# Kernel tuning notes

Measured on AMD Instinct MI355X. Metric: run time of the kernel, lower is better.

## Reference

```python
import jax, jax.numpy as jnp
import numpy as np

N_NODES = 50000
N_EDGES = 800000
D_IN = 128
D_OUT = 128


def setup_inputs() -> dict:
    key = jax.random.key(0)
    k1, k2, k3, k4, k5 = jax.random.split(key, 5)
    x = jax.random.normal(k1, (N_NODES, D_IN), dtype=jnp.float32)
    weight = jax.random.normal(k2, (D_IN, D_OUT), dtype=jnp.float32)
    bias = jax.random.normal(k3, (D_OUT,), dtype=jnp.float32)
    vals = jax.random.uniform(k4, (N_EDGES,), dtype=jnp.float32)
    row = jax.random.randint(k5, (N_EDGES,), 0, N_NODES, dtype=jnp.int32)
    col = jax.random.randint(jax.random.fold_in(k5, 1), (N_EDGES,), 0, N_NODES, dtype=jnp.int32)
    return {"x": x, "weight": weight, "bias": bias, "vals": vals, "row": row, "col": col}


def reference(x, weight, bias, vals, row, col):
    # Dense feature transform: x @ W   [N, D_out]
    h = x @ weight
    # SpMM: out[i] = sum_{e: row[e]==i} vals[e] * h[col[e]]
    msg = vals[:, None] * h[col]  # [E, D_out]
    out = jax.ops.segment_sum(msg, row, num_segments=N_NODES)
    # Fused bias + ReLU (original: out += bias; relu(out))
    out = jax.nn.relu(out + bias)
    return out
```

## Files before the change

### kernel.cpp

```cpp
#include <hip/hip_runtime.h>

#define N_NODES 50000
#define N_EDGES 800000
#define D 128
#define D4 32
#define D2 64

#define BIN_LOG 6
#define BIN_ROWS 64
#define NBINS ((N_NODES + BIN_ROWS - 1) / BIN_ROWS)
#define CAP 1280

#define CNT_STRIDE 16

#define NKEYS 512

#define GEMM_BLOCKS ((N_NODES + 63) / 64)
#define EPB 4096
#define PART_BLOCKS ((N_EDGES + EPB - 1) / EPB)
#define E4 (N_EDGES / 4)

typedef __attribute__((ext_vector_type(8))) short bf16x8;
typedef __attribute__((ext_vector_type(4))) float f32x4;

__device__ __forceinline__ unsigned bf16_1(float a) {
    unsigned u = __float_as_uint(a);
    return (u + 0x7fffu + ((u >> 16) & 1u)) >> 16;
}
__device__ __forceinline__ unsigned pack_bf16(float a, float b) {
    return bf16_1(a) | (bf16_1(b) << 16);
}
__device__ __forceinline__ float ubf_lo(unsigned u) {
    return __uint_as_float(u << 16);
}
__device__ __forceinline__ float ubf_hi(unsigned u) {
    return __uint_as_float(u & 0xffff0000u);
}

__global__ __launch_bounds__(256) void prep_and_zero(const float* __restrict__ w,
                                                     unsigned* __restrict__ wtu,
                                                     int4* __restrict__ cnt4) {
    const int i = blockIdx.x * 256 + threadIdx.x;
    if (i < (NBINS * CNT_STRIDE) / 4) cnt4[i] = make_int4(0, 0, 0, 0);
    if (i < D * 64) {
        const int col = i >> 6;
        const int k2  = i & 63;
        wtu[i] = pack_bf16(w[(size_t)(2 * k2) * D + col],
                           w[(size_t)(2 * k2 + 1) * D + col]);
    }
}

__global__ __launch_bounds__(256) void fused_gemm_partition(
        const float4* __restrict__ x4, const uint4* __restrict__ wt4,
        ushort* __restrict__ hb,
        const int4* __restrict__ rowi4, const int4* __restrict__ coli4,
        const float4* __restrict__ vals4,
        int* __restrict__ bin_cnt, uint2* __restrict__ bins) {

    if (blockIdx.x < PART_BLOCKS) {
        __shared__ int hist[NBINS];
        __shared__ int bbase[NBINS];
        const int base4 = blockIdx.x * (EPB / 4);

        for (int i = threadIdx.x; i < NBINS; i += 256) hist[i] = 0;
        __syncthreads();

        union { int4 v4[4]; int a[16]; } R, C;
        union { float4 v4[4]; float a[16]; } V;
        #pragma unroll
        for (int q = 0; q < 4; ++q) {
            const int i4  = base4 + q * 256 + threadIdx.x;
            const int i4c = (i4 < E4) ? i4 : (E4 - 1);
            R.v4[q] = rowi4[i4c];
            C.v4[q] = coli4[i4c];
            V.v4[q] = vals4[i4c];
            if (i4 >= E4) R.v4[q] = make_int4(-1, -1, -1, -1);
        }

        #pragma unroll
        for (int q = 0; q < 16; ++q)
            if (R.a[q] >= 0) atomicAdd(&hist[R.a[q] >> BIN_LOG], 1);
        __syncthreads();

        for (int i = threadIdx.x; i < NBINS; i += 256) {
            const int c = hist[i];
            bbase[i] = (c > 0) ? atomicAdd(&bin_cnt[i * CNT_STRIDE], c) : 0;
            hist[i] = 0;
        }
        __syncthreads();

        #pragma unroll
        for (int q = 0; q < 16; ++q) {
            const int r = R.a[q];
            if (r >= 0) {
                const int b = r >> BIN_LOG;
                const int k = bbase[b] + atomicAdd(&hist[b], 1);
                const unsigned c = (unsigned)C.a[q];
                if (k < CAP)
                    bins[(size_t)b * CAP + k] =
                        make_uint2((c << 16) | bf16_1(V.a[q]),
                                   ((unsigned)(r & (BIN_ROWS - 1)) << 3) | (c >> 13));
            }
        }
        return;
    }

    const int bid  = blockIdx.x - PART_BLOCKS;
    const int lane = threadIdx.x & 63;
    const int r0   = bid * 64 + (threadIdx.x >> 6) * 16;
    const int arow = r0 + (lane & 15);
    const int kg   = lane >> 4;
    const bool rok = (arow < N_NODES);

    bf16x8 afr[4];
    #pragma unroll
    for (int kc = 0; kc < 4; ++kc) {
        float4 f0 = make_float4(0.f, 0.f, 0.f, 0.f);
        float4 f1 = f0;
        if (rok) {
            const int c4 = kc * 8 + kg * 2;
            f0 = x4[(size_t)arow * D4 + c4];
            f1 = x4[(size_t)arow * D4 + c4 + 1];
        }
        union { bf16x8 v; unsigned u[4]; } a;
        a.u[0] = pack_bf16(f0.x, f0.y);
        a.u[1] = pack_bf16(f0.z, f0.w);
        a.u[2] = pack_bf16(f1.x, f1.y);
        a.u[3] = pack_bf16(f1.z, f1.w);
        afr[kc] = a.v;
    }

    f32x4 acc[8];
    #pragma unroll
    for (int t = 0; t < 8; ++t) acc[t] = (f32x4){0.f, 0.f, 0.f, 0.f};

    #pragma unroll
    for (int t = 0; t < 8; ++t) {
        const int col = t * 16 + (lane & 15);
        #pragma unroll
        for (int kc = 0; kc < 4; ++kc) {
            union { bf16x8 v; uint4 u; } b;
            b.u = wt4[(size_t)col * 16 + kc * 4 + kg];
            acc[t] = __builtin_amdgcn_mfma_f32_16x16x32_bf16(afr[kc], b.v,
                                                             acc[t], 0, 0, 0);
        }
    }

    #pragma unroll
    for (int t = 0; t < 8; ++t) {
        const int col = t * 16 + (lane & 15);
        #pragma unroll
        for (int j = 0; j < 4; ++j) {
            const int r = r0 + (lane >> 4) * 4 + j;
            if (r < N_NODES)
                hb[(size_t)r * D + col] = (ushort)bf16_1(acc[t][j]);
        }
    }
}

__global__ __launch_bounds__(512) void sort_gather(const int* __restrict__ bin_cnt,
                                                   const uint2* __restrict__ bins,
                                                   const uint2* __restrict__ hb2,
                                                   const float4* __restrict__ bias4,
                                                   float4* __restrict__ out4) {
    __shared__ int      hcnt[NKEYS];
    __shared__ int      cur[NKEYS];
    __shared__ int      starts[NKEYS + 1];
    __shared__ int      wsum[8], woff[8];
    __shared__ unsigned sorted[CAP];

    const int bin = blockIdx.x;
    const int tid = threadIdx.x;
    int n = bin_cnt[bin * CNT_STRIDE];
    n = (n > CAP) ? CAP : n;
    const uint2* brec = bins + (size_t)bin * CAP;

    if (tid < NKEYS) { hcnt[tid] = 0; cur[tid] = 0; }
    __syncthreads();

    for (int i = tid; i < n; i += 512) atomicAdd(&hcnt[brec[i].y], 1);
    __syncthreads();

    {
        int v = hcnt[tid];
        #pragma unroll
        for (int off = 1; off < 64; off <<= 1) {
            const int t = __shfl_up(v, off);
            if ((tid & 63) >= off) v += t;
        }
        starts[tid + 1] = v;
        if ((tid & 63) == 63) wsum[tid >> 6] = v;
    }
    __syncthreads();
    if (tid == 0) {
        int run = 0;
        #pragma unroll
        for (int w2 = 0; w2 < 8; ++w2) { woff[w2] = run; run += wsum[w2]; }
        starts[0] = 0;
    }
    __syncthreads();
    starts[tid + 1] += woff[tid >> 6];
    __syncthreads();

    for (int i = tid; i < n; i += 512) {
        const uint2 rec = brec[i];
        const int k = atomicAdd(&cur[rec.y], 1);
        sorted[starts[rec.y] + k] = rec.x;
    }
    __syncthreads();

    const int wave = tid >> 6;
    const int lane = tid & 63;
    const int half = lane >> 5;
    const int hl   = lane & 31;
    const float4 b = bias4[hl];

    #pragma unroll
    for (int rp = 0; rp < 4; ++rp) {
        const int row  = wave + 16 * rp + 8 * half;
        const int node = bin * BIN_ROWS + row;
        int s = 0, len = 0;
        if (node < N_NODES) {
            s   = starts[row << 3];
            len = starts[(row << 3) + 8] - s;
        }
        int lm = len;
        lm = max(lm, __shfl_xor(lm, 32));

        float4 acc = {0.f, 0.f, 0.f, 0.f};
        for (int j0 = 0; j0 < lm; j0 += 8) {
            uint2 hv[8];
            float vv[8];
            #pragma unroll
            for (int q = 0; q < 8; ++q) {
                const int jq = j0 + q;
                const int jj = (jq < len) ? (s + jq) : 0;
                unsigned ed = sorted[jj];
                ed = (jq < len) ? ed : 0u;
                vv[q] = __uint_as_float((ed & 0xffffu) << 16);
                hv[q] = hb2[(size_t)(ed >> 16) * 32 + hl];
            }
            #pragma unroll
            for (int q = 0; q < 8; ++q) {
                acc.x = fmaf(vv[q], ubf_lo(hv[q].x), acc.x);
                acc.y = fmaf(vv[q], ubf_hi(hv[q].x), acc.y);
                acc.z = fmaf(vv[q], ubf_lo(hv[q].y), acc.z);
                acc.w = fmaf(vv[q], ubf_hi(hv[q].y), acc.w);
            }
        }
        if (node < N_NODES) {
            float4 o;
            o.x = fmaxf(acc.x + b.x, 0.f);
            o.y = fmaxf(acc.y + b.y, 0.f);
            o.z = fmaxf(acc.z + b.z, 0.f);
            o.w = fmaxf(acc.w + b.w, 0.f);
            out4[(size_t)node * 32 + hl] = o;
        }
    }
}

extern "C" void kernel_launch(void* const* d_in, const int* in_sizes, int n_in,
                              void* d_out, int out_size, void* d_ws, size_t ws_size,
                              hipStream_t stream) {
    const float* x      = (const float*)d_in[0];
    const float* weight = (const float*)d_in[1];
    const float* bias   = (const float*)d_in[2];
    const float* vals   = (const float*)d_in[3];
    const int*   rowi   = (const int*)d_in[4];
    const int*   coli   = (const int*)d_in[5];
    float* out = (float*)d_out;

    char* w = (char*)d_ws;
    ushort*   hb      = (ushort*)w;   w += (size_t)N_NODES * D * sizeof(ushort);
    unsigned* wt      = (unsigned*)w; w += (size_t)D * 64 * sizeof(unsigned);
    int*      bin_cnt = (int*)w;      w += ((size_t)NBINS * CNT_STRIDE + 16) * sizeof(int);
    uint2*    bins    = (uint2*)w;

    prep_and_zero<<<32, 256, 0, stream>>>(weight, wt, (int4*)bin_cnt);

    fused_gemm_partition<<<PART_BLOCKS + GEMM_BLOCKS, 256, 0, stream>>>(
        (const float4*)x, (const uint4*)wt, hb,
        (const int4*)rowi, (const int4*)coli, (const float4*)vals,
        bin_cnt, bins);

    sort_gather<<<NBINS, 512, 0, stream>>>(bin_cnt, bins, (const uint2*)hb,
                                           (const float4*)bias, (float4*)out);
}
```

Before: 73.39 us.

## Replace global atomic edge binning with per-chunk local sort and bin gather

Each edge chunk is now counting-sorted by bin entirely in shared memory and written out contiguously, along with per-chunk bin start offsets. The sort_gather kernel scans those offsets across all chunks, prefix-sums them, and uses a binary search to fetch its records. This removes the global atomics on bin counters and the zeroing pass, and splits the fused GEMM/partition launch into two separate kernels. In exchange, every bin block reads a strided offset per chunk and does a binary search per record, partition and GEMM no longer overlap within one launch, and bins larger than CAP are no longer clamped.

```diff
diff --git a/kernel.cpp b/kernel.cpp
--- a/kernel.cpp
+++ b/kernel.cpp
@@ -11,14 +11,13 @@
 #define NBINS ((N_NODES + BIN_ROWS - 1) / BIN_ROWS)
 #define CAP 1280
 
-#define CNT_STRIDE 16
-
 #define NKEYS 512
 
+#define EPB 4096
+#define NCHUNK ((N_EDGES + EPB - 1) / EPB)
 #define GEMM_BLOCKS ((N_NODES + 63) / 64)
-#define EPB 4096
-#define PART_BLOCKS ((N_EDGES + EPB - 1) / EPB)
 #define E4 (N_EDGES / 4)
+#define STRIDE_ST (NBINS + 2)
 
 typedef __attribute__((ext_vector_type(8))) short bf16x8;
 typedef __attribute__((ext_vector_type(4))) float f32x4;
@@ -37,11 +36,9 @@
     return __uint_as_float(u & 0xffff0000u);
 }
 
-__global__ __launch_bounds__(256) void prep_and_zero(const float* __restrict__ w,
-                                                     unsigned* __restrict__ wtu,
-                                                     int4* __restrict__ cnt4) {
+__global__ __launch_bounds__(256) void prep_wt(const float* __restrict__ w,
+                                               unsigned* __restrict__ wtu) {
     const int i = blockIdx.x * 256 + threadIdx.x;
-    if (i < (NBINS * CNT_STRIDE) / 4) cnt4[i] = make_int4(0, 0, 0, 0);
     if (i < D * 64) {
         const int col = i >> 6;
         const int k2  = i & 63;
@@ -50,64 +47,96 @@
     }
 }
 
-__global__ __launch_bounds__(256) void fused_gemm_partition(
-        const float4* __restrict__ x4, const uint4* __restrict__ wt4,
-        ushort* __restrict__ hb,
+__global__ __launch_bounds__(256) void partition_edges(
         const int4* __restrict__ rowi4, const int4* __restrict__ coli4,
         const float4* __restrict__ vals4,
-        int* __restrict__ bin_cnt, uint2* __restrict__ bins) {
-
-    if (blockIdx.x < PART_BLOCKS) {
-        __shared__ int hist[NBINS];
-        __shared__ int bbase[NBINS];
-        const int base4 = blockIdx.x * (EPB / 4);
-
-        for (int i = threadIdx.x; i < NBINS; i += 256) hist[i] = 0;
-        __syncthreads();
-
-        union { int4 v4[4]; int a[16]; } R, C;
-        union { float4 v4[4]; float a[16]; } V;
-        #pragma unroll
-        for (int q = 0; q < 4; ++q) {
-            const int i4  = base4 + q * 256 + threadIdx.x;
-            const int i4c = (i4 < E4) ? i4 : (E4 - 1);
-            R.v4[q] = rowi4[i4c];
-            C.v4[q] = coli4[i4c];
-            V.v4[q] = vals4[i4c];
-            if (i4 >= E4) R.v4[q] = make_int4(-1, -1, -1, -1);
-        }
-
-        #pragma unroll
-        for (int q = 0; q < 16; ++q)
-            if (R.a[q] >= 0) atomicAdd(&hist[R.a[q] >> BIN_LOG], 1);
-        __syncthreads();
-
-        for (int i = threadIdx.x; i < NBINS; i += 256) {
-            const int c = hist[i];
-            bbase[i] = (c > 0) ? atomicAdd(&bin_cnt[i * CNT_STRIDE], c) : 0;
-            hist[i] = 0;
-        }
-        __syncthreads();
-
-        #pragma unroll
-        for (int q = 0; q < 16; ++q) {
-            const int r = R.a[q];
-            if (r >= 0) {
-                const int b = r >> BIN_LOG;
-                const int k = bbase[b] + atomicAdd(&hist[b], 1);
-                const unsigned c = (unsigned)C.a[q];
-                if (k < CAP)
-                    bins[(size_t)b * CAP + k] =
-                        make_uint2((c << 16) | bf16_1(V.a[q]),
-                                   ((unsigned)(r & (BIN_ROWS - 1)) << 3) | (c >> 13));
-            }
-        }
-        return;
-    }
-
-    const int bid  = blockIdx.x - PART_BLOCKS;
+        uint2* __restrict__ blk_rec, ushort* __restrict__ blk_starts) {
+    __shared__ int   hist[NBINS];
+    __shared__ int   sts[NBINS + 1];
+    __shared__ int   wsum[4], woff[4];
+    __shared__ uint2 recs[EPB];
+    const int tid = threadIdx.x;
+
+    for (int i = tid; i < NBINS; i += 256) hist[i] = 0;
+    __syncthreads();
+
+    union { int4 v4[4]; int a[16]; } R, C;
+    union { float4 v4[4]; float a[16]; } V;
+    const int base4 = blockIdx.x * (EPB / 4);
+    #pragma unroll
+    for (int q = 0; q < 4; ++q) {
+        const int i4  = base4 + q * 256 + tid;
+        const int i4c = (i4 < E4) ? i4 : (E4 - 1);
+        R.v4[q] = rowi4[i4c];
+        C.v4[q] = coli4[i4c];
+        V.v4[q] = vals4[i4c];
+        if (i4 >= E4) R.v4[q] = make_int4(-1, -1, -1, -1);
+    }
+
+    #pragma unroll
+    for (int q = 0; q < 16; ++q)
+        if (R.a[q] >= 0) atomicAdd(&hist[R.a[q] >> BIN_LOG], 1);
+    __syncthreads();
+
+    int h[4];
+    const int t4 = tid * 4;
+    #pragma unroll
+    for (int k = 0; k < 4; ++k) {
+        const int idx = t4 + k;
+        h[k] = (idx < NBINS) ? hist[idx] : 0;
+    }
+    const int s = h[0] + h[1] + h[2] + h[3];
+    int v = s;
+    #pragma unroll
+    for (int off = 1; off < 64; off <<= 1) {
+        const int t = __shfl_up(v, off);
+        if ((tid & 63) >= off) v += t;
+    }
+    if ((tid & 63) == 63) wsum[tid >> 6] = v;
+    __syncthreads();
+    if (tid == 0) {
+        int run = 0;
+        #pragma unroll
+        for (int w2 = 0; w2 < 4; ++w2) { woff[w2] = run; run += wsum[w2]; }
+    }
+    __syncthreads();
+    int run = woff[tid >> 6] + (v - s);
+    #pragma unroll
+    for (int k = 0; k < 4; ++k) {
+        const int idx = t4 + k;
+        if (idx < NBINS) { sts[idx] = run; run += h[k]; }
+    }
+    if (t4 <= NBINS && NBINS < t4 + 4) sts[NBINS] = run;
+    __syncthreads();
+
+    for (int i = tid; i < NBINS; i += 256) hist[i] = sts[i];
+    __syncthreads();
+
+    #pragma unroll
+    for (int q = 0; q < 16; ++q) {
+        const int r = R.a[q];
+        if (r >= 0) {
+            const int b = r >> BIN_LOG;
+            const int k = atomicAdd(&hist[b], 1);
+            const unsigned c = (unsigned)C.a[q];
+            recs[k] = make_uint2((c << 16) | bf16_1(V.a[q]),
+                                 ((unsigned)(r & (BIN_ROWS - 1)) << 3) | (c >> 13));
+        }
+    }
+    __syncthreads();
+
+    uint4* dst = (uint4*)(blk_rec + (size_t)blockIdx.x * EPB);
+    const uint4* src = (const uint4*)recs;
+    for (int i = tid; i < EPB / 2; i += 256) dst[i] = src[i];
+    ushort* st = blk_starts + (size_t)blockIdx.x * STRIDE_ST;
+    for (int i = tid; i <= NBINS; i += 256) st[i] = (ushort)sts[i];
+}
+
+__global__ __launch_bounds__(256) void gemm_mfma(const float4* __restrict__ x4,
+                                                 const uint4* __restrict__ wt4,
+                                                 ushort* __restrict__ hb) {
     const int lane = threadIdx.x & 63;
-    const int r0   = bid * 64 + (threadIdx.x >> 6) * 16;
+    const int r0   = blockIdx.x * 64 + (threadIdx.x >> 6) * 16;
     const int arow = r0 + (lane & 15);
     const int kg   = lane >> 4;
     const bool rok = (arow < N_NODES);
@@ -158,11 +187,13 @@
     }
 }
 
-__global__ __launch_bounds__(512) void sort_gather(const int* __restrict__ bin_cnt,
-                                                   const uint2* __restrict__ bins,
+__global__ __launch_bounds__(512) void sort_gather(const ushort* __restrict__ blk_starts,
+                                                   const uint2* __restrict__ blk_rec,
                                                    const uint2* __restrict__ hb2,
                                                    const float4* __restrict__ bias4,
                                                    float4* __restrict__ out4) {
+    __shared__ int      chunk_s[NCHUNK];
+    __shared__ int      chunkoff[NCHUNK + 1];
     __shared__ int      hcnt[NKEYS];
     __shared__ int      cur[NKEYS];
     __shared__ int      starts[NKEYS + 1];
@@ -171,23 +202,60 @@
 
     const int bin = blockIdx.x;
     const int tid = threadIdx.x;
-    int n = bin_cnt[bin * CNT_STRIDE];
-    n = (n > CAP) ? CAP : n;
-    const uint2* brec = bins + (size_t)bin * CAP;
-
+
+    int cnt_c = 0;
+    if (tid < NCHUNK) {
+        const ushort* st = blk_starts + (size_t)tid * STRIDE_ST;
+        const int s0 = st[bin];
+        cnt_c = st[bin + 1] - s0;
+        chunk_s[tid] = s0;
+    }
     if (tid < NKEYS) { hcnt[tid] = 0; cur[tid] = 0; }
-    __syncthreads();
-
-    for (int i = tid; i < n; i += 512) atomicAdd(&hcnt[brec[i].y], 1);
-    __syncthreads();
-
-    {
-        int v = hcnt[tid];
+    if (tid < 256) {
+        int v = cnt_c;
         #pragma unroll
         for (int off = 1; off < 64; off <<= 1) {
             const int t = __shfl_up(v, off);
             if ((tid & 63) >= off) v += t;
         }
+        if ((tid & 63) == 63) wsum[tid >> 6] = v;
+        __syncthreads();
+        if (tid == 0) {
+            int run = 0;
+            #pragma unroll
+            for (int w2 = 0; w2 < 4; ++w2) { woff[w2] = run; run += wsum[w2]; }
+        }
+        __syncthreads();
+        if (tid <= NCHUNK) chunkoff[tid] = woff[tid >> 6] + v - cnt_c;
+    } else {
+        __syncthreads();
+        __syncthreads();
+    }
+    __syncthreads();
+    const int n = chunkoff[NCHUNK];
+
+    uint2 rec[3];
+    int nrec = 0;
+    for (int i = tid; i < n; i += 512) {
+        int lo = 0, hi = NCHUNK;
+        while (hi - lo > 1) {
+            const int mid = (lo + hi) >> 1;
+            if (chunkoff[mid] <= i) lo = mid; else hi = mid;
+        }
+        const int slot = i - chunkoff[lo];
+        rec[nrec++] = blk_rec[(size_t)lo * EPB + chunk_s[lo] + slot];
+    }
+
+    for (int k = 0; k < nrec; ++k) atomicAdd(&hcnt[rec[k].y & (NKEYS - 1)], 1);
+    __syncthreads();
+
+    {
+        int v = hcnt[tid];
+        #pragma unroll
+        for (int off = 1; off < 64; off <<= 1) {
+            const int t = __shfl_up(v, off);
+            if ((tid & 63) >= off) v += t;
+        }
         starts[tid + 1] = v;
         if ((tid & 63) == 63) wsum[tid >> 6] = v;
     }
@@ -202,10 +270,10 @@
     starts[tid + 1] += woff[tid >> 6];
     __syncthreads();
 
-    for (int i = tid; i < n; i += 512) {
-        const uint2 rec = brec[i];
-        const int k = atomicAdd(&cur[rec.y], 1);
-        sorted[starts[rec.y] + k] = rec.x;
+    for (int k = 0; k < nrec; ++k) {
+        const int key = rec[k].y & (NKEYS - 1);
+        const int p = atomicAdd(&cur[key], 1);
+        sorted[starts[key] + p] = rec[k].x;
     }
     __syncthreads();
 
@@ -271,18 +339,19 @@
     float* out = (float*)d_out;
 
     char* w = (char*)d_ws;
-    ushort*   hb      = (ushort*)w;   w += (size_t)N_NODES * D * sizeof(ushort);
-    unsigned* wt      = (unsigned*)w; w += (size_t)D * 64 * sizeof(unsigned);
-    int*      bin_cnt = (int*)w;      w += ((size_t)NBINS * CNT_STRIDE + 16) * sizeof(int);
-    uint2*    bins    = (uint2*)w;
-
-    prep_and_zero<<<32, 256, 0, stream>>>(weight, wt, (int4*)bin_cnt);
-
-    fused_gemm_partition<<<PART_BLOCKS + GEMM_BLOCKS, 256, 0, stream>>>(
-        (const float4*)x, (const uint4*)wt, hb,
-        (const int4*)rowi, (const int4*)coli, (const float4*)vals,
-        bin_cnt, bins);
-
-    sort_gather<<<NBINS, 512, 0, stream>>>(bin_cnt, bins, (const uint2*)hb,
+    ushort*   hb         = (ushort*)w;   w += (size_t)N_NODES * D * sizeof(ushort);
+    unsigned* wt         = (unsigned*)w; w += (size_t)D * 64 * sizeof(unsigned);
+    uint2*    blk_rec    = (uint2*)w;    w += (size_t)NCHUNK * EPB * sizeof(uint2);
+    ushort*   blk_starts = (ushort*)w;
+
+    prep_wt<<<32, 256, 0, stream>>>(weight, wt);
+
+    partition_edges<<<NCHUNK, 256, 0, stream>>>((const int4*)rowi, (const int4*)coli,
+                                                (const float4*)vals,
+                                                blk_rec, blk_starts);
+
+    gemm_mfma<<<GEMM_BLOCKS, 256, 0, stream>>>((const float4*)x, (const uint4*)wt, hb);
+
+    sort_gather<<<NBINS, 512, 0, stream>>>(blk_starts, blk_rec, (const uint2*)hb,
                                            (const float4*)bias, (float4*)out);
 }
```

After: 85.84 us. 1.17x slower.

## Replace global atomic bin counters with per-chunk fixed-capacity edge cells

Applied to the files above, without the earlier changes.

The edge partition no longer reserves slots through global atomics on per-bin counters. Each partition block now writes its edges into its own fixed slot (24 records) per bin, plus a per-chunk count table, and the counter-zeroing step is gone. The gather kernel copies every bin's full cell array into shared memory and skips empty slots using the counts. This trades the global atomics and the extra histogram pass for reading a padded buffer several times larger than the real edge data and using more shared memory per block. Edges are silently dropped if any chunk puts more than 24 edges into one bin.

```diff
diff --git a/kernel.cpp b/kernel.cpp
--- a/kernel.cpp
+++ b/kernel.cpp
@@ -4,21 +4,22 @@
 #define N_EDGES 800000
 #define D 128
 #define D4 32
-#define D2 64
 
 #define BIN_LOG 6
 #define BIN_ROWS 64
 #define NBINS ((N_NODES + BIN_ROWS - 1) / BIN_ROWS)
 #define CAP 1280
 
-#define CNT_STRIDE 16
-
 #define NKEYS 512
 
+#define EPB 4096
+#define NCHUNK ((N_EDGES + EPB - 1) / EPB)
 #define GEMM_BLOCKS ((N_NODES + 63) / 64)
-#define EPB 4096
-#define PART_BLOCKS ((N_EDGES + EPB - 1) / EPB)
 #define E4 (N_EDGES / 4)
+
+#define CAP_CELL 24
+#define CELLS_PER_BIN (NCHUNK * CAP_CELL)
+#define CNTROW 784
 
 typedef __attribute__((ext_vector_type(8))) short bf16x8;
 typedef __attribute__((ext_vector_type(4))) float f32x4;
@@ -37,11 +38,9 @@
     return __uint_as_float(u & 0xffff0000u);
 }
 
-__global__ __launch_bounds__(256) void prep_and_zero(const float* __restrict__ w,
-                                                     unsigned* __restrict__ wtu,
-                                                     int4* __restrict__ cnt4) {
+__global__ __launch_bounds__(256) void prep_wt(const float* __restrict__ w,
+                                               unsigned* __restrict__ wtu) {
     const int i = blockIdx.x * 256 + threadIdx.x;
-    if (i < (NBINS * CNT_STRIDE) / 4) cnt4[i] = make_int4(0, 0, 0, 0);
     if (i < D * 64) {
         const int col = i >> 6;
         const int k2  = i & 63;
@@ -50,26 +49,25 @@
     }
 }
 
-__global__ __launch_bounds__(256) void fused_gemm_partition(
+__global__ __launch_bounds__(256) void fused_partition_gemm(
         const float4* __restrict__ x4, const uint4* __restrict__ wt4,
         ushort* __restrict__ hb,
         const int4* __restrict__ rowi4, const int4* __restrict__ coli4,
         const float4* __restrict__ vals4,
-        int* __restrict__ bin_cnt, uint2* __restrict__ bins) {
-
-    if (blockIdx.x < PART_BLOCKS) {
-        __shared__ int hist[NBINS];
-        __shared__ int bbase[NBINS];
-        const int base4 = blockIdx.x * (EPB / 4);
-
-        for (int i = threadIdx.x; i < NBINS; i += 256) hist[i] = 0;
+        uint2* __restrict__ cells, ushort* __restrict__ cnt_t) {
+
+    if (blockIdx.x < NCHUNK) {
+        __shared__ int cur[NBINS];
+        const int tid = threadIdx.x;
+        for (int i = tid; i < NBINS; i += 256) cur[i] = 0;
         __syncthreads();
 
         union { int4 v4[4]; int a[16]; } R, C;
         union { float4 v4[4]; float a[16]; } V;
+        const int base4 = blockIdx.x * (EPB / 4);
         #pragma unroll
         for (int q = 0; q < 4; ++q) {
-            const int i4  = base4 + q * 256 + threadIdx.x;
+            const int i4  = base4 + q * 256 + tid;
             const int i4c = (i4 < E4) ? i4 : (E4 - 1);
             R.v4[q] = rowi4[i4c];
             C.v4[q] = coli4[i4c];
@@ -78,34 +76,27 @@
         }
 
         #pragma unroll
-        for (int q = 0; q < 16; ++q)
-            if (R.a[q] >= 0) atomicAdd(&hist[R.a[q] >> BIN_LOG], 1);
-        __syncthreads();
-
-        for (int i = threadIdx.x; i < NBINS; i += 256) {
-            const int c = hist[i];
-            bbase[i] = (c > 0) ? atomicAdd(&bin_cnt[i * CNT_STRIDE], c) : 0;
-            hist[i] = 0;
-        }
-        __syncthreads();
-
-        #pragma unroll
         for (int q = 0; q < 16; ++q) {
             const int r = R.a[q];
             if (r >= 0) {
                 const int b = r >> BIN_LOG;
-                const int k = bbase[b] + atomicAdd(&hist[b], 1);
+                const int k = atomicAdd(&cur[b], 1);
                 const unsigned c = (unsigned)C.a[q];
-                if (k < CAP)
-                    bins[(size_t)b * CAP + k] =
+                if (k < CAP_CELL)
+                    cells[((size_t)b * NCHUNK + blockIdx.x) * CAP_CELL + k] =
                         make_uint2((c << 16) | bf16_1(V.a[q]),
                                    ((unsigned)(r & (BIN_ROWS - 1)) << 3) | (c >> 13));
             }
         }
+        __syncthreads();
+
+        ushort* ct = cnt_t + (size_t)blockIdx.x * CNTROW;
+        for (int i = tid; i < NBINS; i += 256)
+            ct[i] = (ushort)min(cur[i], CAP_CELL);
         return;
     }
 
-    const int bid  = blockIdx.x - PART_BLOCKS;
+    const int bid  = blockIdx.x - NCHUNK;
     const int lane = threadIdx.x & 63;
     const int r0   = bid * 64 + (threadIdx.x >> 6) * 16;
     const int arow = r0 + (lane & 15);
@@ -158,11 +149,13 @@
     }
 }
 
-__global__ __launch_bounds__(512) void sort_gather(const int* __restrict__ bin_cnt,
-                                                   const uint2* __restrict__ bins,
+__global__ __launch_bounds__(512) void sort_gather(const ushort* __restrict__ cnt_t,
+                                                   const uint2* __restrict__ cells,
                                                    const uint2* __restrict__ hb2,
                                                    const float4* __restrict__ bias4,
                                                    float4* __restrict__ out4) {
+    __shared__ ushort   cnt_c[NCHUNK];
+    __shared__ uint2    raw[CELLS_PER_BIN];
     __shared__ int      hcnt[NKEYS];
     __shared__ int      cur[NKEYS];
     __shared__ int      starts[NKEYS + 1];
@@ -171,14 +164,22 @@
 
     const int bin = blockIdx.x;
     const int tid = threadIdx.x;
-    int n = bin_cnt[bin * CNT_STRIDE];
-    n = (n > CAP) ? CAP : n;
-    const uint2* brec = bins + (size_t)bin * CAP;
-
+
+    if (tid < NCHUNK) cnt_c[tid] = cnt_t[(size_t)tid * CNTROW + bin];
     if (tid < NKEYS) { hcnt[tid] = 0; cur[tid] = 0; }
-    __syncthreads();
-
-    for (int i = tid; i < n; i += 512) atomicAdd(&hcnt[brec[i].y], 1);
+
+    {
+        const uint4* src = (const uint4*)(cells + (size_t)bin * CELLS_PER_BIN);
+        uint4* dst = (uint4*)raw;
+        for (int i = tid; i < CELLS_PER_BIN / 2; i += 512) dst[i] = src[i];
+    }
+    __syncthreads();
+
+    for (int i = tid; i < CELLS_PER_BIN; i += 512) {
+        const int c = i / CAP_CELL;
+        const int s = i - c * CAP_CELL;
+        if (s < (int)cnt_c[c]) atomicAdd(&hcnt[raw[i].y & (NKEYS - 1)], 1);
+    }
     __syncthreads();
 
     {
@@ -202,10 +203,15 @@
     starts[tid + 1] += woff[tid >> 6];
     __syncthreads();
 
-    for (int i = tid; i < n; i += 512) {
-        const uint2 rec = brec[i];
-        const int k = atomicAdd(&cur[rec.y], 1);
-        sorted[starts[rec.y] + k] = rec.x;
+    for (int i = tid; i < CELLS_PER_BIN; i += 512) {
+        const int c = i / CAP_CELL;
+        const int s = i - c * CAP_CELL;
+        if (s < (int)cnt_c[c]) {
+            const int key = raw[i].y & (NKEYS - 1);
+            const int p = atomicAdd(&cur[key], 1);
+            const int dst = starts[key] + p;
+            if (dst < CAP) sorted[dst] = raw[i].x;
+        }
     }
     __syncthreads();
 
@@ -271,18 +277,18 @@
     float* out = (float*)d_out;
 
     char* w = (char*)d_ws;
-    ushort*   hb      = (ushort*)w;   w += (size_t)N_NODES * D * sizeof(ushort);
-    unsigned* wt      = (unsigned*)w; w += (size_t)D * 64 * sizeof(unsigned);
-    int*      bin_cnt = (int*)w;      w += ((size_t)NBINS * CNT_STRIDE + 16) * sizeof(int);
-    uint2*    bins    = (uint2*)w;
-
-    prep_and_zero<<<32, 256, 0, stream>>>(weight, wt, (int4*)bin_cnt);
-
-    fused_gemm_partition<<<PART_BLOCKS + GEMM_BLOCKS, 256, 0, stream>>>(
+    ushort*   hb    = (ushort*)w;   w += (size_t)N_NODES * D * sizeof(ushort);
+    unsigned* wt    = (unsigned*)w; w += (size_t)D * 64 * sizeof(unsigned);
+    uint2*    cells = (uint2*)w;    w += (size_t)NBINS * CELLS_PER_BIN * sizeof(uint2);
+    ushort*   cnt_t = (ushort*)w;
+
+    prep_wt<<<32, 256, 0, stream>>>(weight, wt);
+
+    fused_partition_gemm<<<NCHUNK + GEMM_BLOCKS, 256, 0, stream>>>(
         (const float4*)x, (const uint4*)wt, hb,
         (const int4*)rowi, (const int4*)coli, (const float4*)vals,
-        bin_cnt, bins);
-
-    sort_gather<<<NBINS, 512, 0, stream>>>(bin_cnt, bins, (const uint2*)hb,
+        cells, cnt_t);
+
+    sort_gather<<<NBINS, 512, 0, stream>>>(cnt_t, cells, (const uint2*)hb,
                                            (const float4*)bias, (float4*)out);
 }
```

After: 78.64 us. 7.1% more time.
